# Performance work log

Hardware: AMD Instinct MI355X
Metric: run time of the kernel (lower is better)

Reference implementation:

```python
import jax, jax.numpy as jnp
import numpy as np

B, IN, HID, OUT, E, K = 16384, 512, 1024, 512, 16, 4


def setup_inputs() -> dict:
    key = jax.random.key(0)
    k0, k1, k2, k3 = jax.random.split(key, 4)
    return {
        "x": jax.random.normal(k0, (B, IN), jnp.float32),
        "w_gate": jax.random.normal(k1, (IN, E), jnp.float32) * 0.02,
        "w1": jax.random.normal(k2, (E, IN, HID), jnp.float32) * (1.0 / np.sqrt(IN)),
        "b1": jnp.zeros((E, HID), jnp.float32),
        "w2": jax.random.normal(k3, (E, HID, OUT), jnp.float32) * (1.0 / np.sqrt(HID)),
        "b2": jnp.zeros((E, OUT), jnp.float32),
    }


def _top_k_gating(x, w_gate):
    # Eval-mode (no noise) noisy_top_k_gating: logits -> top-(k+1) -> softmax over top-k
    logits = x @ w_gate  # [B, E]
    m = min(K + 1, E)
    top_logits, top_idx = jax.lax.top_k(logits, m)  # [B, m]
    tk_logits = top_logits[:, :K]                    # [B, K]
    tk_idx = top_idx[:, :K]                          # [B, K] int32
    tk_gates = jax.nn.softmax(tk_logits, axis=1)     # softmax over the k selected
    rows = jnp.arange(logits.shape[0])[:, None]
    gates = jnp.zeros_like(logits).at[rows, tk_idx].set(tk_gates)  # sparse [B, E]
    return gates


def reference(x, w_gate, w1, b1, w2, b2):
    # Gating
    gates = _top_k_gating(x, w_gate)  # [B, E], zero for non-selected experts
    # Dispatch/combine: output[b] = sum_e gates[b,e] * MLP_e(x[b]).
    # Torch code only evaluates experts on selected rows; since gates are exactly
    # zero elsewhere, the dense weighted sum below computes identical math.
    y = jnp.zeros((x.shape[0], w2.shape[2]), x.dtype)
    for e in range(E):  # fixed small expert count; each iter is one grouped GEMM pair
        h = jax.nn.relu(x @ w1[e] + b1[e])                 # [B, HID]
        o = jax.nn.softmax(h @ w2[e] + b2[e], axis=1)      # expert MLP ends in Softmax(dim=1)
        y = y + gates[:, e:e + 1] * o
    return y
```

## Files before the change

### kernel.cpp

```cpp
#include <hip/hip_runtime.h>
#include <hip/hip_fp16.h>

typedef _Float16 f16;
typedef _Float16 f16x8 __attribute__((ext_vector_type(8)));
typedef float f32x4 __attribute__((ext_vector_type(4)));

#define MFMA(a,b,c) __builtin_amdgcn_mfma_f32_16x16x32_f16((a),(b),(c),0,0,0)


__global__ void k_cvt_w1(const float* __restrict__ w1, f16* __restrict__ w1fr) {
  int fid = blockIdx.x * 4 + (threadIdx.x >> 6);
  int l = threadIdx.x & 63;
  int e = fid >> 10, n0 = (fid >> 4) & 63, kc = fid & 15;
  int kbase = kc * 32 + (l >> 4) * 8;
  int col = n0 * 16 + (l & 15);
  const float* src = w1 + ((size_t)e * 512 + kbase) * 1024 + col;
  f16x8 o;
  #pragma unroll
  for (int i = 0; i < 8; i++) o[i] = (f16)src[(size_t)i * 1024];
  *(f16x8*)(w1fr + (size_t)fid * 512 + l * 8) = o;
}

__global__ void k_cvt_w2(const float* __restrict__ w2, f16* __restrict__ w2fr) {
  int fid = blockIdx.x * 4 + (threadIdx.x >> 6);
  int l = threadIdx.x & 63;
  int e = fid >> 10, n0 = (fid >> 5) & 31, kc = fid & 31;
  int kbase = kc * 32 + (l >> 4) * 8;
  int col = n0 * 16 + (l & 15);
  const float* src = w2 + ((size_t)e * 1024 + kbase) * 512 + col;
  f16x8 o;
  #pragma unroll
  for (int i = 0; i < 8; i++) o[i] = (f16)src[(size_t)i * 512];
  *(f16x8*)(w2fr + (size_t)fid * 512 + l * 8) = o;
}

__global__ void k_gate(const float* __restrict__ x, const float* __restrict__ wg,
                       int* __restrict__ tk_idx, float* __restrict__ tk_gate) {
  int w = threadIdx.x >> 6, l = threadIdx.x & 63;
  int r = blockIdx.x * 4 + w;
  float p[16];
  #pragma unroll
  for (int e = 0; e < 16; e++) p[e] = 0.f;
  const float* xr = x + (size_t)r * 512;
  #pragma unroll
  for (int t = 0; t < 8; t++) {
    float xv = xr[t * 64 + l];
    const float* wrow = wg + (t * 64 + l) * 16;
    #pragma unroll
    for (int e = 0; e < 16; e++) p[e] += xv * wrow[e];
  }
  #pragma unroll
  for (int e = 0; e < 16; e++) {
    float v = p[e];
    #pragma unroll
    for (int m = 32; m >= 1; m >>= 1) v += __shfl_xor(v, m);
    p[e] = v;
  }
  unsigned chosen = 0;
  float bv[4]; int bi[4];
  #pragma unroll
  for (int j = 0; j < 4; j++) {
    float best = -3.4e38f; int be = 0;
    #pragma unroll
    for (int e = 0; e < 16; e++) {
      bool ok = !((chosen >> e) & 1u) && (p[e] > best);
      if (ok) { best = p[e]; be = e; }
    }
    chosen |= 1u << be; bv[j] = best; bi[j] = be;
  }
  float m0 = bv[0];
  float e0 = __expf(bv[0] - m0), e1 = __expf(bv[1] - m0),
        e2 = __expf(bv[2] - m0), e3 = __expf(bv[3] - m0);
  float s = e0 + e1 + e2 + e3;
  if (l == 0) {
    *(int4*)(tk_idx + (size_t)r * 4) = make_int4(bi[0], bi[1], bi[2], bi[3]);
    *(float4*)(tk_gate + (size_t)r * 4) = make_float4(e0 / s, e1 / s, e2 / s, e3 / s);
  }
}

__global__ void k_route_count(const int* __restrict__ tk_idx, int* __restrict__ partial) {
  int e = blockIdx.x >> 6, chunk = blockIdx.x & 63;
  int t = threadIdx.x;
  int row = chunk * 256 + t;
  int4 tk = ((const int4*)tk_idx)[row];
  bool match = (tk.x == e) || (tk.y == e) || (tk.z == e) || (tk.w == e);
  unsigned long long m = __ballot(match);
  __shared__ int wc[4];
  if ((t & 63) == 0) wc[t >> 6] = (int)__popcll(m);
  __syncthreads();
  if (t == 0) partial[e * 64 + chunk] = wc[0] + wc[1] + wc[2] + wc[3];
}

__global__ void k_route_scan(const int* __restrict__ partial, int* __restrict__ chunk_base,
                             int* __restrict__ count) {
  int l = threadIdx.x;
  for (int e = 0; e < 16; e++) {
    int v = partial[e * 64 + l];
    int orig = v;
    #pragma unroll
    for (int off = 1; off < 64; off <<= 1) {
      int u = __shfl_up(v, off);
      if (l >= off) v += u;
    }
    chunk_base[e * 64 + l] = v - orig;
    if (l == 63) count[e] = v;
  }
}

__global__ void k_route_scatter(const int* __restrict__ tk_idx, const float* __restrict__ tk_gate,
                                const int* __restrict__ chunk_base, int* __restrict__ rows_pk,
                                float* __restrict__ gates_l) {
  int e = blockIdx.x >> 6, chunk = blockIdx.x & 63;
  int t = threadIdx.x, w = t >> 6, l = t & 63;
  int row = chunk * 256 + t;
  int4 tk = ((const int4*)tk_idx)[row];
  int j = (tk.x == e) ? 0 : (tk.y == e) ? 1 : (tk.z == e) ? 2 : (tk.w == e) ? 3 : -1;
  bool match = (j >= 0);
  unsigned long long m = __ballot(match);
  __shared__ int wc[4];
  if (l == 0) wc[w] = (int)__popcll(m);
  __syncthreads();
  int wbase = 0;
  #pragma unroll
  for (int i = 0; i < 4; i++) if (i < w) wbase += wc[i];
  if (match) {
    int pos = (int)__popcll(m & ((1ULL << l) - 1ULL));
    int idx = e * 16384 + chunk_base[e * 64 + chunk] + wbase + pos;
    rows_pk[idx] = row | (j << 16);
    gates_l[idx] = tk_gate[(size_t)row * 4 + j];
  }
}

__global__ void k_zero(float4* __restrict__ y4) {
  y4[blockIdx.x * 256 + threadIdx.x] = make_float4(0.f, 0.f, 0.f, 0.f);
}

__global__ __launch_bounds__(512, 2) void k_expert(
    const float* __restrict__ x, const f16* __restrict__ w1fr, const f16* __restrict__ w2fr,
    const float* __restrict__ b1, const float* __restrict__ b2,
    const int* __restrict__ count, const int* __restrict__ rows_pk,
    const float* __restrict__ gates_l, float* __restrict__ y)
{
  int p = blockIdx.x;
  int xcd = p & 7, s = p >> 3;
  int e = (xcd << 1) | (s >> 8);
  int rb = s & 255;
  int cnt = count[e];
  int mstart = rb * 64;
  if (mstart >= cnt) return;
  int nvalid = cnt - mstart; if (nvalid > 64) nvalid = 64;

  __shared__ f16 x_lds[64 * 128];
  __shared__ f16 h_lds[64 * 256];
  __shared__ int rowarr[64];
  __shared__ float gatearr[64];
  __shared__ float red[2][8][64];

  int t = threadIdx.x, w = t >> 6, l = t & 63;
  int lq = l >> 4, lr = l & 15;

  if (t < 64) {
    int idx = (t < nvalid) ? t : (nvalid - 1);
    int src = e * 16384 + mstart + idx;
    rowarr[t] = rows_pk[src];
    gatearr[t] = gates_l[src];
  }
  __syncthreads();

  int srow = t >> 3, sc0 = (t & 7) * 16;
  const float* sp = x + (size_t)(rowarr[srow] & 0xFFFF) * 512 + sc0;

  const f16x8* w1f8 = (const f16x8*)w1fr;
  const f16x8* w2f8 = (const f16x8*)w2fr;

  f32x4 acc2[4][4];
  #pragma unroll
  for (int a = 0; a < 4; a++)
    #pragma unroll
    for (int b = 0; b < 4; b++)
      #pragma unroll
      for (int q = 0; q < 4; q++) acc2[a][b][q] = 0.f;

  #pragma unroll 1
  for (int hc = 0; hc < 4; hc++) {
    f32x4 acc1[4][2];
    #pragma unroll
    for (int a = 0; a < 4; a++)
      #pragma unroll
      for (int b = 0; b < 2; b++)
        #pragma unroll
        for (int q = 0; q < 4; q++) acc1[a][b][q] = 0.f;

    #pragma unroll 1
    for (int kk = 0; kk < 4; kk++) {
      __syncthreads();
      {
        const float* qp = sp + kk * 128;
        float4 u0 = *(const float4*)(qp + 0);
        float4 u1 = *(const float4*)(qp + 4);
        float4 u2 = *(const float4*)(qp + 8);
        float4 u3 = *(const float4*)(qp + 12);
        f16x8 v0, v1;
        v0[0]=(f16)u0.x; v0[1]=(f16)u0.y; v0[2]=(f16)u0.z; v0[3]=(f16)u0.w;
        v0[4]=(f16)u1.x; v0[5]=(f16)u1.y; v0[6]=(f16)u1.z; v0[7]=(f16)u1.w;
        v1[0]=(f16)u2.x; v1[1]=(f16)u2.y; v1[2]=(f16)u2.z; v1[3]=(f16)u2.w;
        v1[4]=(f16)u3.x; v1[5]=(f16)u3.y; v1[6]=(f16)u3.z; v1[7]=(f16)u3.w;
        int b0 = (srow * 256 + sc0 * 2) ^ ((srow & 7) << 4);
        int b1b = (srow * 256 + sc0 * 2 + 16) ^ ((srow & 7) << 4);
        *(f16x8*)((char*)x_lds + b0) = v0;
        *(f16x8*)((char*)x_lds + b1b) = v1;
      }
      __syncthreads();

      const f16x8* bp1 = w1f8 + ((size_t)((e * 64 + hc * 16 + w * 2) * 16 + kk * 4)) * 64 + l;
      f16x8 bfa0 = bp1[0], bfa1 = bp1[16 * 64];
      #pragma unroll
      for (int k4 = 0; k4 < 4; k4++) {
        f16x8 bfb0, bfb1;
        if (k4 < 3) { bfb0 = bp1[(k4 + 1) * 64]; bfb1 = bp1[16 * 64 + (k4 + 1) * 64]; }
        f16x8 av[4];
        #pragma unroll
        for (int mf = 0; mf < 4; mf++) {
          int row = mf * 16 + lr;
          int byte = (row * 256 + k4 * 64 + lq * 16) ^ ((lr & 7) << 4);
          av[mf] = *(const f16x8*)((char*)x_lds + byte);
        }
        #pragma unroll
        for (int mf = 0; mf < 4; mf++) {
          acc1[mf][0] = MFMA(av[mf], bfa0, acc1[mf][0]);
          acc1[mf][1] = MFMA(av[mf], bfa1, acc1[mf][1]);
        }
        if (k4 < 3) { bfa0 = bfb0; bfa1 = bfb1; }
      }
    }

    __syncthreads();
    #pragma unroll
    for (int nf = 0; nf < 2; nf++) {
      int col = w * 32 + nf * 16 + lr;
      float bv = b1[e * 1024 + hc * 256 + col];
      #pragma unroll
      for (int mf = 0; mf < 4; mf++)
        #pragma unroll
        for (int q = 0; q < 4; q++) {
          int row = mf * 16 + lq * 4 + q;
          float hv = fmaxf(acc1[mf][nf][q] + bv, 0.f);
          int byte = (row * 512 + col * 2) ^ ((row & 7) << 4);
          *(f16*)((char*)h_lds + byte) = (f16)hv;
        }
    }
    __syncthreads();

    const f16x8* bp2 = w2f8 + ((size_t)((e * 32 + w * 4) * 32 + hc * 8)) * 64 + l;
    f16x8 wfa0 = bp2[0 * 2048], wfa1 = bp2[1 * 2048], wfa2 = bp2[2 * 2048], wfa3 = bp2[3 * 2048];
    #pragma unroll
    for (int kc2 = 0; kc2 < 8; kc2++) {
      f16x8 wfb0, wfb1, wfb2, wfb3;
      if (kc2 < 7) {
        wfb0 = bp2[0 * 2048 + (kc2 + 1) * 64];
        wfb1 = bp2[1 * 2048 + (kc2 + 1) * 64];
        wfb2 = bp2[2 * 2048 + (kc2 + 1) * 64];
        wfb3 = bp2[3 * 2048 + (kc2 + 1) * 64];
      }
      f16x8 av[4];
      #pragma unroll
      for (int mf = 0; mf < 4; mf++) {
        int row = mf * 16 + lr;
        int byte = (row * 512 + kc2 * 64 + lq * 16) ^ ((lr & 7) << 4);
        av[mf] = *(const f16x8*)((char*)h_lds + byte);
      }
      #pragma unroll
      for (int mf = 0; mf < 4; mf++) {
        acc2[mf][0] = MFMA(av[mf], wfa0, acc2[mf][0]);
        acc2[mf][1] = MFMA(av[mf], wfa1, acc2[mf][1]);
        acc2[mf][2] = MFMA(av[mf], wfa2, acc2[mf][2]);
        acc2[mf][3] = MFMA(av[mf], wfa3, acc2[mf][3]);
      }
      if (kc2 < 7) { wfa0 = wfb0; wfa1 = wfb1; wfa2 = wfb2; wfa3 = wfb3; }
    }
  }

  #pragma unroll
  for (int nf = 0; nf < 4; nf++) {
    float bv = b2[e * 512 + w * 64 + nf * 16 + lr];
    #pragma unroll
    for (int mf = 0; mf < 4; mf++)
      #pragma unroll
      for (int q = 0; q < 4; q++) acc2[mf][nf][q] += bv;
  }

  float rmax[4][4];
  #pragma unroll
  for (int mf = 0; mf < 4; mf++)
    #pragma unroll
    for (int q = 0; q < 4; q++) {
      float v = acc2[mf][0][q];
      #pragma unroll
      for (int nf = 1; nf < 4; nf++) v = fmaxf(v, acc2[mf][nf][q]);
      #pragma unroll
      for (int m = 1; m < 16; m <<= 1) v = fmaxf(v, __shfl_xor(v, m));
      rmax[mf][q] = v;
    }
  if (lr == 0) {
    #pragma unroll
    for (int mf = 0; mf < 4; mf++)
      #pragma unroll
      for (int q = 0; q < 4; q++) red[0][w][mf * 16 + lq * 4 + q] = rmax[mf][q];
  }
  __syncthreads();
  float gmax[4][4];
  #pragma unroll
  for (int mf = 0; mf < 4; mf++)
    #pragma unroll
    for (int q = 0; q < 4; q++) {
      int row = mf * 16 + lq * 4 + q;
      float v = red[0][0][row];
      #pragma unroll
      for (int ww = 1; ww < 8; ww++) v = fmaxf(v, red[0][ww][row]);
      gmax[mf][q] = v;
    }
  float psum[4][4];
  #pragma unroll
  for (int mf = 0; mf < 4; mf++)
    #pragma unroll
    for (int q = 0; q < 4; q++) psum[mf][q] = 0.f;
  #pragma unroll
  for (int mf = 0; mf < 4; mf++)
    #pragma unroll
    for (int nf = 0; nf < 4; nf++)
      #pragma unroll
      for (int q = 0; q < 4; q++) {
        float pp = __expf(acc2[mf][nf][q] - gmax[mf][q]);
        acc2[mf][nf][q] = pp;
        psum[mf][q] += pp;
      }
  #pragma unroll
  for (int mf = 0; mf < 4; mf++)
    #pragma unroll
    for (int q = 0; q < 4; q++) {
      float v = psum[mf][q];
      #pragma unroll
      for (int m = 1; m < 16; m <<= 1) v += __shfl_xor(v, m);
      psum[mf][q] = v;
    }
  if (lr == 0) {
    #pragma unroll
    for (int mf = 0; mf < 4; mf++)
      #pragma unroll
      for (int q = 0; q < 4; q++) red[1][w][mf * 16 + lq * 4 + q] = psum[mf][q];
  }
  __syncthreads();

  #pragma unroll
  for (int mf = 0; mf < 4; mf++) {
    #pragma unroll
    for (int q = 0; q < 4; q++) {
      int row = mf * 16 + lq * 4 + q;
      if (row < nvalid) {
        float ssum = 0.f;
        #pragma unroll
        for (int ww = 0; ww < 8; ww++) ssum += red[1][ww][row];
        float sc = gatearr[row] / ssum;
        int orow = rowarr[row] & 0xFFFF;
        float* yr = y + (size_t)orow * 512 + w * 64 + lr;
        #pragma unroll
        for (int nf = 0; nf < 4; nf++) {
          atomicAdd(yr + nf * 16, acc2[mf][nf][q] * sc);
        }
      }
    }
  }
}

extern "C" void kernel_launch(void* const* d_in, const int* in_sizes, int n_in,
                              void* d_out, int out_size, void* d_ws, size_t ws_size,
                              hipStream_t stream) {
  (void)in_sizes; (void)n_in; (void)out_size; (void)ws_size;
  const float* x  = (const float*)d_in[0];
  const float* wg = (const float*)d_in[1];
  const float* w1 = (const float*)d_in[2];
  const float* b1 = (const float*)d_in[3];
  const float* w2 = (const float*)d_in[4];
  const float* b2 = (const float*)d_in[5];
  float* y = (float*)d_out;

  char* ws = (char*)d_ws;
  size_t off = 0;
  auto alloc = [&](size_t bytes) -> char* {
    char* p = ws + off;
    off += (bytes + 255) & ~(size_t)255;
    return p;
  };
  f16*   w1fr       = (f16*)  alloc((size_t)16 * 512 * 1024 * 2);
  f16*   w2fr       = (f16*)  alloc((size_t)16 * 1024 * 512 * 2);
  int*   tk_idx     = (int*)  alloc((size_t)16384 * 4 * 4);
  float* tk_gate    = (float*)alloc((size_t)16384 * 4 * 4);
  int*   rows_pk    = (int*)  alloc((size_t)16 * 16384 * 4);
  float* gates_l    = (float*)alloc((size_t)16 * 16384 * 4);
  int*   partial    = (int*)  alloc(16 * 64 * 4);
  int*   chunk_base = (int*)  alloc(16 * 64 * 4);
  int*   count      = (int*)  alloc(256);

  k_cvt_w1<<<dim3(4096), dim3(256), 0, stream>>>(w1, w1fr);
  k_cvt_w2<<<dim3(4096), dim3(256), 0, stream>>>(w2, w2fr);
  k_gate<<<dim3(4096), dim3(256), 0, stream>>>(x, wg, tk_idx, tk_gate);
  k_route_count<<<dim3(1024), dim3(256), 0, stream>>>(tk_idx, partial);
  k_route_scan<<<dim3(1), dim3(64), 0, stream>>>(partial, chunk_base, count);
  k_route_scatter<<<dim3(1024), dim3(256), 0, stream>>>(tk_idx, tk_gate, chunk_base,
                                                        rows_pk, gates_l);
  k_zero<<<dim3(8192), dim3(256), 0, stream>>>((float4*)y);
  k_expert<<<dim3(4096), dim3(512), 0, stream>>>(x, w1fr, w2fr, b1, b2,
                                                 count, rows_pk, gates_l, y);
}
```

Before: 438.7 us.

## Double-buffer x tiles, widen hidden chunk to 512, pad LDS instead of swizzling

The first GEMM now prefetches the next x k-slice from global memory into a second LDS buffer while MFMAs run on the current one, so one barrier per k-step replaces two. The hidden dimension is processed in two chunks of 512 instead of four of 256, which halves how often x is reloaded and widens each wave's first-GEMM output tile. The XOR swizzle on LDS is replaced by padded row strides, and __syncthreads is replaced by an explicit lgkmcnt wait plus s_barrier. In exchange, LDS use per block grows to roughly 100KB and accumulator registers double, which likely prevents the two blocks per CU that the launch bounds request.

```diff
diff --git a/kernel.cpp b/kernel.cpp
--- a/kernel.cpp
+++ b/kernel.cpp
@@ -6,6 +6,13 @@
 typedef float f32x4 __attribute__((ext_vector_type(4)));
 
 #define MFMA(a,b,c) __builtin_amdgcn_mfma_f32_16x16x32_f16((a),(b),(c),0,0,0)
+
+#define BAR() do { \
+  asm volatile("s_waitcnt lgkmcnt(0)" ::: "memory"); \
+  __builtin_amdgcn_sched_barrier(0); \
+  __builtin_amdgcn_s_barrier(); \
+  __builtin_amdgcn_sched_barrier(0); \
+} while (0)
 
 
 __global__ void k_cvt_w1(const float* __restrict__ w1, f16* __restrict__ w1fr) {
@@ -150,8 +157,8 @@
   if (mstart >= cnt) return;
   int nvalid = cnt - mstart; if (nvalid > 64) nvalid = 64;
 
-  __shared__ f16 x_lds[64 * 128];
-  __shared__ f16 h_lds[64 * 256];
+  __shared__ f16 x_lds[2][64 * 136];
+  __shared__ f16 h_lds[64 * 520];
   __shared__ int rowarr[64];
   __shared__ float gatearr[64];
   __shared__ float red[2][8][64];
@@ -165,10 +172,14 @@
     rowarr[t] = rows_pk[src];
     gatearr[t] = gates_l[src];
   }
-  __syncthreads();
+  BAR();
 
   int srow = t >> 3, sc0 = (t & 7) * 16;
   const float* sp = x + (size_t)(rowarr[srow] & 0xFFFF) * 512 + sc0;
+  char* xl0 = (char*)&x_lds[0][0];
+  char* xl1 = (char*)&x_lds[1][0];
+  char* hl  = (char*)h_lds;
+  int xwb = srow * 272 + sc0 * 2;
 
   const f16x8* w1f8 = (const f16x8*)w1fr;
   const f16x8* w2f8 = (const f16x8*)w2fr;
@@ -182,101 +193,116 @@
       for (int q = 0; q < 4; q++) acc2[a][b][q] = 0.f;
 
   #pragma unroll 1
-  for (int hc = 0; hc < 4; hc++) {
-    f32x4 acc1[4][2];
+  for (int hc = 0; hc < 2; hc++) {
+    {
+      const float* qp = sp;
+      float4 u0 = ((const float4*)qp)[0], u1 = ((const float4*)qp)[1];
+      float4 u2 = ((const float4*)qp)[2], u3 = ((const float4*)qp)[3];
+      f16x8 v0, v1;
+      v0[0]=(f16)u0.x; v0[1]=(f16)u0.y; v0[2]=(f16)u0.z; v0[3]=(f16)u0.w;
+      v0[4]=(f16)u1.x; v0[5]=(f16)u1.y; v0[6]=(f16)u1.z; v0[7]=(f16)u1.w;
+      v1[0]=(f16)u2.x; v1[1]=(f16)u2.y; v1[2]=(f16)u2.z; v1[3]=(f16)u2.w;
+      v1[4]=(f16)u3.x; v1[5]=(f16)u3.y; v1[6]=(f16)u3.z; v1[7]=(f16)u3.w;
+      *(f16x8*)(xl0 + xwb) = v0;
+      *(f16x8*)(xl0 + xwb + 16) = v1;
+    }
+    const f16x8* bp1h = w1f8 + ((size_t)((e * 64 + hc * 32 + w * 4) * 16)) * 64 + l;
+    f16x8 ba0 = bp1h[0], ba1 = bp1h[16 * 64], ba2 = bp1h[32 * 64], ba3 = bp1h[48 * 64];
+    BAR();
+
+    f32x4 acc1[4][4];
     #pragma unroll
     for (int a = 0; a < 4; a++)
       #pragma unroll
-      for (int b = 0; b < 2; b++)
+      for (int b = 0; b < 4; b++)
         #pragma unroll
         for (int q = 0; q < 4; q++) acc1[a][b][q] = 0.f;
 
     #pragma unroll 1
     for (int kk = 0; kk < 4; kk++) {
-      __syncthreads();
-      {
-        const float* qp = sp + kk * 128;
-        float4 u0 = *(const float4*)(qp + 0);
-        float4 u1 = *(const float4*)(qp + 4);
-        float4 u2 = *(const float4*)(qp + 8);
-        float4 u3 = *(const float4*)(qp + 12);
+      char* xbuf = (kk & 1) ? xl1 : xl0;
+      char* xnxt = (kk & 1) ? xl0 : xl1;
+      float4 u0, u1, u2, u3;
+      if (kk < 3) {
+        const float* qp = sp + (kk + 1) * 128;
+        u0 = ((const float4*)qp)[0]; u1 = ((const float4*)qp)[1];
+        u2 = ((const float4*)qp)[2]; u3 = ((const float4*)qp)[3];
+      }
+      const f16x8* bp1 = bp1h + (size_t)(kk * 4) * 64;
+      #pragma unroll
+      for (int k4 = 0; k4 < 4; k4++) {
+        f16x8 bb0, bb1, bb2, bb3;
+        if (k4 < 3) {
+          bb0 = bp1[(k4 + 1) * 64];
+          bb1 = bp1[16 * 64 + (k4 + 1) * 64];
+          bb2 = bp1[32 * 64 + (k4 + 1) * 64];
+          bb3 = bp1[48 * 64 + (k4 + 1) * 64];
+        }
+        f16x8 av[4];
+        #pragma unroll
+        for (int mf = 0; mf < 4; mf++)
+          av[mf] = *(const f16x8*)(xbuf + (mf * 16 + lr) * 272 + k4 * 64 + lq * 16);
+        #pragma unroll
+        for (int mf = 0; mf < 4; mf++) {
+          acc1[mf][0] = MFMA(av[mf], ba0, acc1[mf][0]);
+          acc1[mf][1] = MFMA(av[mf], ba1, acc1[mf][1]);
+          acc1[mf][2] = MFMA(av[mf], ba2, acc1[mf][2]);
+          acc1[mf][3] = MFMA(av[mf], ba3, acc1[mf][3]);
+        }
+        if (k4 < 3) { ba0 = bb0; ba1 = bb1; ba2 = bb2; ba3 = bb3; }
+      }
+      if (kk < 3) {
         f16x8 v0, v1;
         v0[0]=(f16)u0.x; v0[1]=(f16)u0.y; v0[2]=(f16)u0.z; v0[3]=(f16)u0.w;
         v0[4]=(f16)u1.x; v0[5]=(f16)u1.y; v0[6]=(f16)u1.z; v0[7]=(f16)u1.w;
         v1[0]=(f16)u2.x; v1[1]=(f16)u2.y; v1[2]=(f16)u2.z; v1[3]=(f16)u2.w;
         v1[4]=(f16)u3.x; v1[5]=(f16)u3.y; v1[6]=(f16)u3.z; v1[7]=(f16)u3.w;
-        int b0 = (srow * 256 + sc0 * 2) ^ ((srow & 7) << 4);
-        int b1b = (srow * 256 + sc0 * 2 + 16) ^ ((srow & 7) << 4);
-        *(f16x8*)((char*)x_lds + b0) = v0;
-        *(f16x8*)((char*)x_lds + b1b) = v1;
-      }
-      __syncthreads();
-
-      const f16x8* bp1 = w1f8 + ((size_t)((e * 64 + hc * 16 + w * 2) * 16 + kk * 4)) * 64 + l;
-      f16x8 bfa0 = bp1[0], bfa1 = bp1[16 * 64];
-      #pragma unroll
-      for (int k4 = 0; k4 < 4; k4++) {
-        f16x8 bfb0, bfb1;
-        if (k4 < 3) { bfb0 = bp1[(k4 + 1) * 64]; bfb1 = bp1[16 * 64 + (k4 + 1) * 64]; }
-        f16x8 av[4];
-        #pragma unroll
-        for (int mf = 0; mf < 4; mf++) {
-          int row = mf * 16 + lr;
-          int byte = (row * 256 + k4 * 64 + lq * 16) ^ ((lr & 7) << 4);
-          av[mf] = *(const f16x8*)((char*)x_lds + byte);
-        }
-        #pragma unroll
-        for (int mf = 0; mf < 4; mf++) {
-          acc1[mf][0] = MFMA(av[mf], bfa0, acc1[mf][0]);
-          acc1[mf][1] = MFMA(av[mf], bfa1, acc1[mf][1]);
-        }
-        if (k4 < 3) { bfa0 = bfb0; bfa1 = bfb1; }
-      }
-    }
-
-    __syncthreads();
-    #pragma unroll
-    for (int nf = 0; nf < 2; nf++) {
-      int col = w * 32 + nf * 16 + lr;
-      float bv = b1[e * 1024 + hc * 256 + col];
+        *(f16x8*)(xnxt + xwb) = v0;
+        *(f16x8*)(xnxt + xwb + 16) = v1;
+        const f16x8* bpn = bp1h + (size_t)((kk + 1) * 4) * 64;
+        ba0 = bpn[0]; ba1 = bpn[16 * 64]; ba2 = bpn[32 * 64]; ba3 = bpn[48 * 64];
+      }
+      BAR();
+    }
+
+    #pragma unroll
+    for (int nf = 0; nf < 4; nf++) {
+      int colc = w * 64 + nf * 16 + lr;
+      float bv = b1[e * 1024 + hc * 512 + colc];
       #pragma unroll
       for (int mf = 0; mf < 4; mf++)
         #pragma unroll
         for (int q = 0; q < 4; q++) {
           int row = mf * 16 + lq * 4 + q;
           float hv = fmaxf(acc1[mf][nf][q] + bv, 0.f);
-          int byte = (row * 512 + col * 2) ^ ((row & 7) << 4);
-          *(f16*)((char*)h_lds + byte) = (f16)hv;
+          *(f16*)(hl + row * 1040 + colc * 2) = (f16)hv;
         }
     }
-    __syncthreads();
-
-    const f16x8* bp2 = w2f8 + ((size_t)((e * 32 + w * 4) * 32 + hc * 8)) * 64 + l;
-    f16x8 wfa0 = bp2[0 * 2048], wfa1 = bp2[1 * 2048], wfa2 = bp2[2 * 2048], wfa3 = bp2[3 * 2048];
-    #pragma unroll
-    for (int kc2 = 0; kc2 < 8; kc2++) {
-      f16x8 wfb0, wfb1, wfb2, wfb3;
-      if (kc2 < 7) {
-        wfb0 = bp2[0 * 2048 + (kc2 + 1) * 64];
-        wfb1 = bp2[1 * 2048 + (kc2 + 1) * 64];
-        wfb2 = bp2[2 * 2048 + (kc2 + 1) * 64];
-        wfb3 = bp2[3 * 2048 + (kc2 + 1) * 64];
+    const f16x8* bp2 = w2f8 + ((size_t)((e * 32 + w * 4) * 32 + hc * 16)) * 64 + l;
+    f16x8 wa0 = bp2[0], wa1 = bp2[32 * 64], wa2 = bp2[64 * 64], wa3 = bp2[96 * 64];
+    BAR();
+
+    #pragma unroll 2
+    for (int kc2 = 0; kc2 < 16; kc2++) {
+      f16x8 wb0, wb1, wb2, wb3;
+      if (kc2 < 15) {
+        wb0 = bp2[(kc2 + 1) * 64];
+        wb1 = bp2[32 * 64 + (kc2 + 1) * 64];
+        wb2 = bp2[64 * 64 + (kc2 + 1) * 64];
+        wb3 = bp2[96 * 64 + (kc2 + 1) * 64];
       }
       f16x8 av[4];
       #pragma unroll
+      for (int mf = 0; mf < 4; mf++)
+        av[mf] = *(const f16x8*)(hl + (mf * 16 + lr) * 1040 + kc2 * 64 + lq * 16);
+      #pragma unroll
       for (int mf = 0; mf < 4; mf++) {
-        int row = mf * 16 + lr;
-        int byte = (row * 512 + kc2 * 64 + lq * 16) ^ ((lr & 7) << 4);
-        av[mf] = *(const f16x8*)((char*)h_lds + byte);
-      }
-      #pragma unroll
-      for (int mf = 0; mf < 4; mf++) {
-        acc2[mf][0] = MFMA(av[mf], wfa0, acc2[mf][0]);
-        acc2[mf][1] = MFMA(av[mf], wfa1, acc2[mf][1]);
-        acc2[mf][2] = MFMA(av[mf], wfa2, acc2[mf][2]);
-        acc2[mf][3] = MFMA(av[mf], wfa3, acc2[mf][3]);
-      }
-      if (kc2 < 7) { wfa0 = wfb0; wfa1 = wfb1; wfa2 = wfb2; wfa3 = wfb3; }
+        acc2[mf][0] = MFMA(av[mf], wa0, acc2[mf][0]);
+        acc2[mf][1] = MFMA(av[mf], wa1, acc2[mf][1]);
+        acc2[mf][2] = MFMA(av[mf], wa2, acc2[mf][2]);
+        acc2[mf][3] = MFMA(av[mf], wa3, acc2[mf][3]);
+      }
+      if (kc2 < 15) { wa0 = wb0; wa1 = wb1; wa2 = wb2; wa3 = wb3; }
     }
   }
 
@@ -307,7 +333,7 @@
       #pragma unroll
       for (int q = 0; q < 4; q++) red[0][w][mf * 16 + lq * 4 + q] = rmax[mf][q];
   }
-  __syncthreads();
+  BAR();
   float gmax[4][4];
   #pragma unroll
   for (int mf = 0; mf < 4; mf++)
@@ -349,7 +375,7 @@
       #pragma unroll
       for (int q = 0; q < 4; q++) red[1][w][mf * 16 + lq * 4 + q] = psum[mf][q];
   }
-  __syncthreads();
+  BAR();
 
   #pragma unroll
   for (int mf = 0; mf < 4; mf++) {
```

Measured after the change: 362.2 us. -17.4%, faster.
